# Optimization experiments

Measured on AMD Instinct MI355X. Metric: run time of the kernel, lower is better.

Reference implementation:

```python
import jax, jax.numpy as jnp
import numpy as np

S, B, H = 2048, 32, 1024

def setup_inputs() -> dict:
    key = jax.random.key(0)
    k1, k2, k3 = jax.random.split(key, 3)
    hidden = jax.random.normal(k1, (1, B, H), dtype=jnp.float32)
    encoder_outputs = jax.random.normal(k2, (S, B, H), dtype=jnp.float32)
    W = jax.random.normal(k3, (H, H), dtype=jnp.float32) * (1.0 / np.sqrt(H))
    b = jnp.zeros((H,), dtype=jnp.float32)
    return {"hidden": hidden, "encoder_outputs": encoder_outputs, "W": W, "b": b}

def reference(hidden, encoder_outputs, W, b):
    # method == 'general': energy[b,i] = hidden[0,b] . (W @ enc[i,b] + bias)
    # proj: [S, B, H] = enc @ W^T + b  (nn.Linear convention: y = x W^T + b)
    proj = jnp.einsum('sbh,kh->sbk', encoder_outputs, W) + b
    # scores: [B, S]
    scores = jnp.einsum('bh,sbh->bs', hidden[0], proj)
    attn = jax.nn.softmax(scores, axis=1)
    return attn[:, None, :]  # [B, 1, S]
```

## Files before the change

### kernel.cpp

```cpp
#include <hip/hip_runtime.h>
#include <math.h>

#define H 1024
#define S 2048
#define B 32

__global__ void __launch_bounds__(512)
proj_hidden_kernel(const float* __restrict__ hidden,
                   const float* __restrict__ W,
                   float* __restrict__ v) {
    __shared__ float hs[H];
    __shared__ float part[3][128];
    const int b  = blockIdx.x >> 3;
    const int hc = blockIdx.x & 7;
    const int hl = threadIdx.x & 127;
    const int kg = threadIdx.x >> 7;
    const int h  = hc * 128 + hl;

    for (int i = threadIdx.x; i < H; i += 512) hs[i] = hidden[b * H + i];
    __syncthreads();

    const int k0 = kg * 256;
    const float* Wp = W + (size_t)k0 * H + h;
    float a0 = 0.f, a1 = 0.f, a2 = 0.f, a3 = 0.f;
#pragma unroll 4
    for (int k = 0; k < 256; k += 4) {
        a0 = fmaf(hs[k0 + k + 0], Wp[(size_t)(k + 0) * H], a0);
        a1 = fmaf(hs[k0 + k + 1], Wp[(size_t)(k + 1) * H], a1);
        a2 = fmaf(hs[k0 + k + 2], Wp[(size_t)(k + 2) * H], a2);
        a3 = fmaf(hs[k0 + k + 3], Wp[(size_t)(k + 3) * H], a3);
    }
    float acc = (a0 + a1) + (a2 + a3);

    if (kg > 0) part[kg - 1][hl] = acc;
    __syncthreads();
    if (kg == 0) {
        acc += part[0][hl] + part[1][hl] + part[2][hl];
        v[b * H + h] = acc;
    }
}

__global__ void __launch_bounds__(256)
scores_kernel(const float* __restrict__ enc,
              const float* __restrict__ v,
              float* __restrict__ scores) {
    const int s0 = blockIdx.x * 2;
    const int b  = threadIdx.x >> 3;
    const int k  = threadIdx.x & 7;

    const float4* e0 = reinterpret_cast<const float4*>(enc + ((size_t)s0 * B + b) * H);
    const float4* e1 = reinterpret_cast<const float4*>(enc + ((size_t)(s0 + 1) * B + b) * H);
    const float4* vb = reinterpret_cast<const float4*>(v + (size_t)b * H);

    float acc0 = 0.f, acc1 = 0.f;
#pragma unroll 4
    for (int j = 0; j < 32; ++j) {
        const int f = k + 8 * j;
        const float4 w = vb[f];
        const float4 x = e0[f];
        const float4 y = e1[f];
        acc0 = fmaf(x.x, w.x, fmaf(x.y, w.y, fmaf(x.z, w.z, fmaf(x.w, w.w, acc0))));
        acc1 = fmaf(y.x, w.x, fmaf(y.y, w.y, fmaf(y.z, w.z, fmaf(y.w, w.w, acc1))));
    }
#pragma unroll
    for (int off = 4; off > 0; off >>= 1) {
        acc0 += __shfl_down(acc0, off, 8);
        acc1 += __shfl_down(acc1, off, 8);
    }
    if (k == 0) {
        scores[(size_t)b * S + s0]     = acc0;
        scores[(size_t)b * S + s0 + 1] = acc1;
    }
}

__global__ void __launch_bounds__(256)
softmax_kernel(const float* __restrict__ scores,
               float* __restrict__ out) {
    const int b    = blockIdx.x;
    const int tid  = threadIdx.x;
    const int wave = tid >> 6;
    const int lane = tid & 63;

    __shared__ float wmax[4];
    __shared__ float wsum[4];

    float x[8];
    float m = -INFINITY;
#pragma unroll
    for (int i = 0; i < 8; ++i) {
        x[i] = scores[(size_t)b * S + tid + i * 256];
        m = fmaxf(m, x[i]);
    }
#pragma unroll
    for (int off = 32; off > 0; off >>= 1)
        m = fmaxf(m, __shfl_down(m, off, 64));
    if (lane == 0) wmax[wave] = m;
    __syncthreads();
    m = fmaxf(fmaxf(wmax[0], wmax[1]), fmaxf(wmax[2], wmax[3]));

    float sum = 0.f;
#pragma unroll
    for (int i = 0; i < 8; ++i) {
        x[i] = __expf(x[i] - m);
        sum += x[i];
    }
#pragma unroll
    for (int off = 32; off > 0; off >>= 1)
        sum += __shfl_down(sum, off, 64);
    if (lane == 0) wsum[wave] = sum;
    __syncthreads();
    sum = (wsum[0] + wsum[1]) + (wsum[2] + wsum[3]);

    const float inv = 1.0f / sum;
#pragma unroll
    for (int i = 0; i < 8; ++i) {
        out[(size_t)b * S + tid + i * 256] = x[i] * inv;
    }
}

extern "C" void kernel_launch(void* const* d_in, const int* in_sizes, int n_in,
                              void* d_out, int out_size, void* d_ws, size_t ws_size,
                              hipStream_t stream) {
    const float* hidden = (const float*)d_in[0];
    const float* enc    = (const float*)d_in[1];
    const float* W      = (const float*)d_in[2];

    float* v      = (float*)d_ws;
    float* scores = v + (size_t)B * H;
    float* out    = (float*)d_out;

    proj_hidden_kernel<<<B * 8, 512, 0, stream>>>(hidden, W, v);
    scores_kernel<<<S / 2, 256, 0, stream>>>(enc, v, scores);
    softmax_kernel<<<B, 256, 0, stream>>>(scores, out);
}
```

Measured before the change: 58.67 us.

## Reuse W rows across two batches with float4 loads; process four positions per scores block

```diff
diff --git a/kernel.cpp b/kernel.cpp
--- a/kernel.cpp
+++ b/kernel.cpp
@@ -9,34 +9,42 @@
 proj_hidden_kernel(const float* __restrict__ hidden,
                    const float* __restrict__ W,
                    float* __restrict__ v) {
-    __shared__ float hs[H];
-    __shared__ float part[3][128];
-    const int b  = blockIdx.x >> 3;
-    const int hc = blockIdx.x & 7;
-    const int hl = threadIdx.x & 127;
-    const int kg = threadIdx.x >> 7;
-    const int h  = hc * 128 + hl;
+    __shared__ float hs[2][H];
+    __shared__ float part[32][2][64];
+    const int hc = blockIdx.x & 15;
+    const int bg = blockIdx.x >> 4;
+    const int hq = threadIdx.x & 15;
+    const int kg = threadIdx.x >> 4;
 
-    for (int i = threadIdx.x; i < H; i += 512) hs[i] = hidden[b * H + i];
+    for (int i = threadIdx.x; i < 2 * H; i += 512)
+        hs[i >> 10][i & 1023] = hidden[(bg * 2 + (i >> 10)) * H + (i & 1023)];
     __syncthreads();
 
-    const int k0 = kg * 256;
-    const float* Wp = W + (size_t)k0 * H + h;
-    float a0 = 0.f, a1 = 0.f, a2 = 0.f, a3 = 0.f;
+    const int h = hc * 64 + hq * 4;
+    float4 a0 = {0.f, 0.f, 0.f, 0.f};
+    float4 a1 = {0.f, 0.f, 0.f, 0.f};
 #pragma unroll 4
-    for (int k = 0; k < 256; k += 4) {
-        a0 = fmaf(hs[k0 + k + 0], Wp[(size_t)(k + 0) * H], a0);
-        a1 = fmaf(hs[k0 + k + 1], Wp[(size_t)(k + 1) * H], a1);
-        a2 = fmaf(hs[k0 + k + 2], Wp[(size_t)(k + 2) * H], a2);
-        a3 = fmaf(hs[k0 + k + 3], Wp[(size_t)(k + 3) * H], a3);
+    for (int kk = 0; kk < 32; ++kk) {
+        const int k = kg + 32 * kk;
+        const float h0 = hs[0][k];
+        const float h1 = hs[1][k];
+        const float4 w = *reinterpret_cast<const float4*>(W + (size_t)k * H + h);
+        a0.x = fmaf(h0, w.x, a0.x); a0.y = fmaf(h0, w.y, a0.y);
+        a0.z = fmaf(h0, w.z, a0.z); a0.w = fmaf(h0, w.w, a0.w);
+        a1.x = fmaf(h1, w.x, a1.x); a1.y = fmaf(h1, w.y, a1.y);
+        a1.z = fmaf(h1, w.z, a1.z); a1.w = fmaf(h1, w.w, a1.w);
     }
-    float acc = (a0 + a1) + (a2 + a3);
+    *reinterpret_cast<float4*>(&part[kg][0][hq * 4]) = a0;
+    *reinterpret_cast<float4*>(&part[kg][1][hq * 4]) = a1;
+    __syncthreads();
 
-    if (kg > 0) part[kg - 1][hl] = acc;
-    __syncthreads();
-    if (kg == 0) {
-        acc += part[0][hl] + part[1][hl] + part[2][hl];
-        v[b * H + h] = acc;
+    if (threadIdx.x < 128) {
+        const int bb = threadIdx.x >> 6;
+        const int c  = threadIdx.x & 63;
+        float sum = 0.f;
+#pragma unroll 8
+        for (int g = 0; g < 32; ++g) sum += part[g][bb][c];
+        v[(bg * 2 + bb) * H + hc * 64 + c] = sum;
     }
 }
 
@@ -44,32 +52,40 @@
 scores_kernel(const float* __restrict__ enc,
               const float* __restrict__ v,
               float* __restrict__ scores) {
-    const int s0 = blockIdx.x * 2;
+    const int s0 = blockIdx.x * 4;
     const int b  = threadIdx.x >> 3;
     const int k  = threadIdx.x & 7;
 
-    const float4* e0 = reinterpret_cast<const float4*>(enc + ((size_t)s0 * B + b) * H);
+    const float4* e0 = reinterpret_cast<const float4*>(enc + ((size_t)(s0 + 0) * B + b) * H);
     const float4* e1 = reinterpret_cast<const float4*>(enc + ((size_t)(s0 + 1) * B + b) * H);
+    const float4* e2 = reinterpret_cast<const float4*>(enc + ((size_t)(s0 + 2) * B + b) * H);
+    const float4* e3 = reinterpret_cast<const float4*>(enc + ((size_t)(s0 + 3) * B + b) * H);
     const float4* vb = reinterpret_cast<const float4*>(v + (size_t)b * H);
 
-    float acc0 = 0.f, acc1 = 0.f;
+    float a0 = 0.f, a1 = 0.f, a2 = 0.f, a3 = 0.f;
 #pragma unroll 4
     for (int j = 0; j < 32; ++j) {
         const int f = k + 8 * j;
         const float4 w = vb[f];
-        const float4 x = e0[f];
-        const float4 y = e1[f];
-        acc0 = fmaf(x.x, w.x, fmaf(x.y, w.y, fmaf(x.z, w.z, fmaf(x.w, w.w, acc0))));
-        acc1 = fmaf(y.x, w.x, fmaf(y.y, w.y, fmaf(y.z, w.z, fmaf(y.w, w.w, acc1))));
+        const float4 x0 = e0[f];
+        const float4 x1 = e1[f];
+        const float4 x2 = e2[f];
+        const float4 x3 = e3[f];
+        a0 = fmaf(x0.x, w.x, fmaf(x0.y, w.y, fmaf(x0.z, w.z, fmaf(x0.w, w.w, a0))));
+        a1 = fmaf(x1.x, w.x, fmaf(x1.y, w.y, fmaf(x1.z, w.z, fmaf(x1.w, w.w, a1))));
+        a2 = fmaf(x2.x, w.x, fmaf(x2.y, w.y, fmaf(x2.z, w.z, fmaf(x2.w, w.w, a2))));
+        a3 = fmaf(x3.x, w.x, fmaf(x3.y, w.y, fmaf(x3.z, w.z, fmaf(x3.w, w.w, a3))));
     }
 #pragma unroll
     for (int off = 4; off > 0; off >>= 1) {
-        acc0 += __shfl_down(acc0, off, 8);
-        acc1 += __shfl_down(acc1, off, 8);
+        a0 += __shfl_down(a0, off, 8);
+        a1 += __shfl_down(a1, off, 8);
+        a2 += __shfl_down(a2, off, 8);
+        a3 += __shfl_down(a3, off, 8);
     }
     if (k == 0) {
-        scores[(size_t)b * S + s0]     = acc0;
-        scores[(size_t)b * S + s0 + 1] = acc1;
+        float* sp = scores + (size_t)b * S + s0;
+        sp[0] = a0; sp[1] = a1; sp[2] = a2; sp[3] = a3;
     }
 }
 
@@ -129,7 +145,7 @@
     float* scores = v + (size_t)B * H;
     float* out    = (float*)d_out;
 
-    proj_hidden_kernel<<<B * 8, 512, 0, stream>>>(hidden, W, v);
-    scores_kernel<<<S / 2, 256, 0, stream>>>(enc, v, scores);
+    proj_hidden_kernel<<<256, 512, 0, stream>>>(hidden, W, v);
+    scores_kernel<<<S / 4, 256, 0, stream>>>(enc, v, scores);
     softmax_kernel<<<B, 256, 0, stream>>>(scores, out);
 }
```

Result: faster. 54.58 us (-7.0%).
